# Optimization experiments

Hardware: AMD Instinct MI355X
Metric: run time of the kernel (lower is better)

Reference implementation:

```python
import jax, jax.numpy as jnp
import numpy as np


def setup_inputs() -> dict:
    key = jax.random.key(0)
    kx, km = jax.random.split(key)
    B, T, D = 32, 4096, 512
    x = jax.random.normal(kx, (B, T, D), dtype=jnp.float32)
    # mask semantics follow the torch module: True = excluded, kept rows are ~mask
    mask = jax.random.randint(km, (B, T), 0, 2) == 1
    # ensure at least one kept (False) position per row so mean is well-defined
    mask = mask.at[:, 0].set(False)
    return {"x": x, "mask": mask}


def reference(x, mask):
    # masked mean over time: keep positions where mask is False (torch uses v[~m])
    keep = (~mask).astype(x.dtype)                      # [B, T]
    denom = jnp.sum(keep, axis=1, keepdims=True)        # [B, 1]
    pooled = jnp.einsum('btd,bt->bd', x, keep) / denom  # [B, D]
    return pooled
```

## Files before the change

kernel.cpp:

```cpp
#include <hip/hip_runtime.h>


#define BB 32
#define TT 4096
#define DD 512
#define SPLITS 64
#define ROWS (TT / SPLITS)
#define D4 (DD / 4)

__global__ __launch_bounds__(128) void masked_pool_partial(
    const float* __restrict__ x, const int* __restrict__ mask,
    float4* __restrict__ ws)
{
    __shared__ float s_keep[ROWS];
    const int b   = blockIdx.x;
    const int s   = blockIdx.y;
    const int tid = threadIdx.x;
    const int t0  = s * ROWS;

    if (tid < ROWS)
        s_keep[tid] = (mask[b * TT + t0 + tid] == 0) ? 1.0f : 0.0f;
    __syncthreads();

    const float4* xp = (const float4*)x + ((size_t)b * TT + t0) * D4 + tid;

    float4 acc = make_float4(0.f, 0.f, 0.f, 0.f);
    #pragma unroll 8
    for (int r = 0; r < ROWS; ++r) {
        const float  k = s_keep[r];
        const float4 v = xp[(size_t)r * D4];
        acc.x += k * v.x;
        acc.y += k * v.y;
        acc.z += k * v.z;
        acc.w += k * v.w;
    }

    ws[((size_t)b * SPLITS + s) * D4 + tid] = acc;
}

__global__ __launch_bounds__(256) void masked_pool_reduce(
    const float4* __restrict__ ws, const int* __restrict__ mask,
    float4* __restrict__ out)
{
    const int b   = blockIdx.x;
    const int tid = threadIdx.x;

    int cnt = 0;
    #pragma unroll
    for (int t = tid; t < TT; t += 256) cnt += (mask[b * TT + t] == 0) ? 1 : 0;
    #pragma unroll
    for (int off = 32; off > 0; off >>= 1) cnt += __shfl_down(cnt, off, 64);

    __shared__ int s_cnt[4];
    if ((tid & 63) == 0) s_cnt[tid >> 6] = cnt;
    __syncthreads();
    const float inv = 1.0f / (float)(s_cnt[0] + s_cnt[1] + s_cnt[2] + s_cnt[3]);

    if (tid < D4) {
        const float4* p = ws + (size_t)b * SPLITS * D4 + tid;
        float4 acc = make_float4(0.f, 0.f, 0.f, 0.f);
        #pragma unroll 8
        for (int s = 0; s < SPLITS; ++s) {
            const float4 v = p[(size_t)s * D4];
            acc.x += v.x; acc.y += v.y; acc.z += v.z; acc.w += v.w;
        }
        acc.x *= inv; acc.y *= inv; acc.z *= inv; acc.w *= inv;
        out[(size_t)b * D4 + tid] = acc;
    }
}

extern "C" void kernel_launch(void* const* d_in, const int* in_sizes, int n_in,
                              void* d_out, int out_size, void* d_ws, size_t ws_size,
                              hipStream_t stream) {
    const float* x    = (const float*)d_in[0];
    const int*   mask = (const int*)d_in[1];
    float4*      ws   = (float4*)d_ws;
    float4*      out  = (float4*)d_out;

    dim3 grid(BB, SPLITS);
    masked_pool_partial<<<grid, 128, 0, stream>>>(x, mask, ws);
    masked_pool_reduce<<<BB, 256, 0, stream>>>(ws, mask, out);
}
```

Before: 372.0 us.

## Fuse partial and reduce kernels via last-block atomic counter

Merges the two-kernel split reduction into one kernel. Each block writes its partial sum, bumps a per-batch atomic counter, and the last block to arrive for a batch reduces all partials and applies the mask count. This removes the second kernel launch and its dependency gap, at the cost of an extra memset, fences and an atomic per block. The inner loop unroll also goes from 8 to 16.

```diff
diff --git a/kernel.cpp b/kernel.cpp
--- a/kernel.cpp
+++ b/kernel.cpp
@@ -8,11 +8,15 @@
 #define ROWS (TT / SPLITS)
 #define D4 (DD / 4)
 
-__global__ __launch_bounds__(128) void masked_pool_partial(
+__global__ __launch_bounds__(128) void masked_pool_fused(
     const float* __restrict__ x, const int* __restrict__ mask,
-    float4* __restrict__ ws)
+    float4* __restrict__ ws, int* __restrict__ cnt,
+    float4* __restrict__ out)
 {
     __shared__ float s_keep[ROWS];
+    __shared__ int   s_red[2];
+    __shared__ int   s_last;
+
     const int b   = blockIdx.x;
     const int s   = blockIdx.y;
     const int tid = threadIdx.x;
@@ -25,7 +29,7 @@
     const float4* xp = (const float4*)x + ((size_t)b * TT + t0) * D4 + tid;
 
     float4 acc = make_float4(0.f, 0.f, 0.f, 0.f);
-    #pragma unroll 8
+    #pragma unroll 16
     for (int r = 0; r < ROWS; ++r) {
         const float  k = s_keep[r];
         const float4 v = xp[(size_t)r * D4];
@@ -36,37 +40,36 @@
     }
 
     ws[((size_t)b * SPLITS + s) * D4 + tid] = acc;
-}
 
-__global__ __launch_bounds__(256) void masked_pool_reduce(
-    const float4* __restrict__ ws, const int* __restrict__ mask,
-    float4* __restrict__ out)
-{
-    const int b   = blockIdx.x;
-    const int tid = threadIdx.x;
+    __threadfence();
+    if (tid == 0) {
+        const int old = atomicAdd(&cnt[b], 1);
+        s_last = (old == SPLITS - 1) ? 1 : 0;
+    }
+    __syncthreads();
+    if (!s_last) return;
 
-    int cnt = 0;
+    __threadfence();
+
+    const float4* p = ws + (size_t)b * SPLITS * D4 + tid;
+    float4 r = make_float4(0.f, 0.f, 0.f, 0.f);
+    #pragma unroll 8
+    for (int k = 0; k < SPLITS; ++k) {
+        const float4 v = p[(size_t)k * D4];
+        r.x += v.x; r.y += v.y; r.z += v.z; r.w += v.w;
+    }
+
+    int c = 0;
     #pragma unroll
-    for (int t = tid; t < TT; t += 256) cnt += (mask[b * TT + t] == 0) ? 1 : 0;
+    for (int t = tid; t < TT; t += 128) c += (mask[b * TT + t] == 0) ? 1 : 0;
     #pragma unroll
-    for (int off = 32; off > 0; off >>= 1) cnt += __shfl_down(cnt, off, 64);
+    for (int off = 32; off > 0; off >>= 1) c += __shfl_down(c, off, 64);
+    if ((tid & 63) == 0) s_red[tid >> 6] = c;
+    __syncthreads();
+    const float inv = 1.0f / (float)(s_red[0] + s_red[1]);
 
-    __shared__ int s_cnt[4];
-    if ((tid & 63) == 0) s_cnt[tid >> 6] = cnt;
-    __syncthreads();
-    const float inv = 1.0f / (float)(s_cnt[0] + s_cnt[1] + s_cnt[2] + s_cnt[3]);
-
-    if (tid < D4) {
-        const float4* p = ws + (size_t)b * SPLITS * D4 + tid;
-        float4 acc = make_float4(0.f, 0.f, 0.f, 0.f);
-        #pragma unroll 8
-        for (int s = 0; s < SPLITS; ++s) {
-            const float4 v = p[(size_t)s * D4];
-            acc.x += v.x; acc.y += v.y; acc.z += v.z; acc.w += v.w;
-        }
-        acc.x *= inv; acc.y *= inv; acc.z *= inv; acc.w *= inv;
-        out[(size_t)b * D4 + tid] = acc;
-    }
+    r.x *= inv; r.y *= inv; r.z *= inv; r.w *= inv;
+    out[(size_t)b * D4 + tid] = r;
 }
 
 extern "C" void kernel_launch(void* const* d_in, const int* in_sizes, int n_in,
@@ -74,10 +77,14 @@
                               hipStream_t stream) {
     const float* x    = (const float*)d_in[0];
     const int*   mask = (const int*)d_in[1];
-    float4*      ws   = (float4*)d_ws;
     float4*      out  = (float4*)d_out;
 
+    const size_t part_bytes = (size_t)BB * SPLITS * D4 * sizeof(float4);
+    float4* ws_part = (float4*)d_ws;
+    int*    ws_cnt  = (int*)((char*)d_ws + part_bytes);
+
+    hipMemsetAsync(ws_cnt, 0, BB * sizeof(int), stream);
+
     dim3 grid(BB, SPLITS);
-    masked_pool_partial<<<grid, 128, 0, stream>>>(x, mask, ws);
-    masked_pool_reduce<<<BB, 256, 0, stream>>>(ws, mask, out);
+    masked_pool_fused<<<grid, 128, 0, stream>>>(x, mask, ws_part, ws_cnt, out);
 }
```

Result: slower. 552.9 us (+48.6%).
